# Optimization experiments

Hardware: AMD Instinct MI355X
Metric: run time of the kernel (lower is better)

Reference implementation:

```python
import jax, jax.numpy as jnp
import numpy as np
from functools import partial

D_MODEL = 1024
D_STATE = 16
D_CONV = 4
EXPAND = 2
DIM = EXPAND * D_MODEL  # 2048


def setup_inputs() -> dict:
    key = jax.random.key(0)
    ks = jax.random.split(key, 10)
    s = lambda fan_in: 1.0 / np.sqrt(fan_in)
    inp = {
        "x": jax.random.normal(ks[0], (8, 2048, D_MODEL), dtype=jnp.float32),
        "W_in": jax.random.normal(ks[1], (DIM, D_MODEL), dtype=jnp.float32) * s(D_MODEL),
        "b_in": jnp.zeros((DIM,), dtype=jnp.float32),
        "conv_w": jax.random.normal(ks[2], (DIM, 1, D_CONV), dtype=jnp.float32) * s(D_CONV),
        "conv_b": jnp.zeros((DIM,), dtype=jnp.float32),
        "W_x": jax.random.normal(ks[3], (3 * D_STATE, DIM), dtype=jnp.float32) * s(DIM),
        "W_dt": jax.random.normal(ks[4], (DIM, D_STATE), dtype=jnp.float32) * s(D_STATE),
        "b_dt": jnp.zeros((DIM,), dtype=jnp.float32),
        "W_out": jax.random.normal(ks[5], (D_MODEL, DIM), dtype=jnp.float32) * s(DIM),
        "b_out": jnp.zeros((D_MODEL,), dtype=jnp.float32),
    }
    return inp


def _selective_scan(xc, delta, A, Bm, Cm):
    # xc, delta: (B, L, DIM); Bm, Cm: (B, L, N); A: (N,)
    Bsz = xc.shape[0]
    h0 = jnp.zeros((Bsz, DIM, D_STATE), dtype=xc.dtype)

    def step(h, inputs):
        xc_t, d_t, b_t, c_t = inputs  # (B,DIM),(B,DIM),(B,N),(B,N)
        h = h * jnp.exp(d_t[:, :, None] * A) + xc_t[:, :, None] * b_t[:, None, :]
        y_t = jnp.einsum("bdn,bn->bd", h, c_t)
        return h, y_t

    tm = lambda a: jnp.swapaxes(a, 0, 1)  # time-major
    _, ys = jax.lax.scan(step, h0, (tm(xc), tm(delta), tm(Bm), tm(Cm)))
    return jnp.swapaxes(ys, 0, 1)  # (B, L, DIM)


def reference(x, W_in, b_in, conv_w, conv_b, W_x, W_dt, b_dt, W_out, b_out):
    A = -jnp.exp(jnp.linspace(0.0, -5.0, D_STATE).astype(x.dtype))  # (N,)
    xp = x @ W_in.T + b_in  # (B, L, DIM)
    # depthwise conv1d, padding=D_CONV-1 on BOTH sides (as torch Conv1d) -> length L+D_CONV-1
    xc = jax.lax.conv_general_dilated(
        jnp.swapaxes(xp, 1, 2), conv_w,
        window_strides=(1,), padding=[(D_CONV - 1, D_CONV - 1)],
        feature_group_count=DIM,
        dimension_numbers=("NCH", "OIH", "NCH"),
    ) + conv_b[None, :, None]
    xc = jnp.swapaxes(xc, 1, 2)  # (B, Lc, DIM)
    x_dbl = xc @ W_x.T  # (B, Lc, 3N)
    d_raw, Bm, Cm = jnp.split(x_dbl, [D_STATE, 2 * D_STATE], axis=-1)
    delta = jax.nn.softplus(d_raw @ W_dt.T + b_dt)  # (B, Lc, DIM)
    y = _selective_scan(xc, delta, A, Bm, Cm)  # (B, Lc, DIM)
    return y @ W_out.T + b_out  # (B, Lc, D_MODEL)
```

## Files before the change

kernel.cpp:

```cpp
#include <hip/hip_runtime.h>
#include <cstdint>
#include <cstddef>

#define B8 8
#define LSEQ 2048
#define LC 2051
#define DMODEL 1024
#define DIM 2048
#define LPAD 2054
#define M2 16408
#define M2P 16512
#define CS 32
#define NCH 65

typedef __attribute__((ext_vector_type(8))) short short8;
typedef __attribute__((ext_vector_type(4))) float floatx4;
typedef __attribute__((ext_vector_type(2))) float float2v;

__device__ __constant__ float AeT[16] = {
  -1.0f,          -0.71653131f, -0.51341712f, -0.36787944f,
  -0.26359714f,   -0.18887560f, -0.13533528f, -0.09697208f,
  -0.06948345f,   -0.04978707f, -0.03567399f, -0.02556154f,
  -0.01831564f,   -0.01312373f, -0.00940356f, -0.00673795f};

#define LOG2E 1.44269504088896f

__device__ __forceinline__ float bf2f(unsigned short h) {
  union { unsigned int u; float f; } v; v.u = ((unsigned int)h) << 16; return v.f;
}
__device__ __forceinline__ unsigned short f2bf(float f) {
  union { float f; unsigned int u; } v; v.f = f;
  unsigned int r = (v.u + 0x7FFFu + ((v.u >> 16) & 1u)) >> 16;
  return (unsigned short)r;
}

__device__ __forceinline__ float2v pk_mul_vv(float2v a, float2v b) {
  float2v d; asm("v_pk_mul_f32 %0, %1, %2" : "=v"(d) : "v"(a), "v"(b)); return d;
}
__device__ __forceinline__ float2v pk_mul_sv(float2v bs, float2v a) {
  float2v d; asm("v_pk_mul_f32 %0, %1, %2" : "=v"(d) : "s"(bs), "v"(a)); return d;
}
__device__ __forceinline__ float2v pk_fma_vvv(float2v a, float2v b, float2v c) {
  float2v d; asm("v_pk_fma_f32 %0, %1, %2, %3" : "=v"(d) : "v"(a), "v"(b), "v"(c)); return d;
}
__device__ __forceinline__ float2v pk_fma_vsv(float2v a, float2v bs, float2v c) {
  float2v d; asm("v_pk_fma_f32 %0, %1, %2, %3" : "=v"(d) : "v"(a), "s"(bs), "v"(c)); return d;
}
__device__ __forceinline__ float2v pk_add_vv(float2v a, float2v b) {
  float2v d; asm("v_pk_add_f32 %0, %1, %2" : "=v"(d) : "v"(a), "v"(b)); return d;
}
__device__ __forceinline__ float exp2_raw(float x) {
  float d; asm("v_exp_f32 %0, %1" : "=v"(d) : "v"(x)); return d;
}

__global__ __launch_bounds__(256) void cvt_f32_bf16(const float* __restrict__ in,
                                                    unsigned short* __restrict__ out,
                                                    int n8) {
  int i = blockIdx.x * 256 + threadIdx.x;
  if (i >= n8) return;
  const float4* p = (const float4*)in + (size_t)i * 2;
  float4 a = p[0], b = p[1];
  uint4 o;
  o.x = (unsigned)f2bf(a.x) | ((unsigned)f2bf(a.y) << 16);
  o.y = (unsigned)f2bf(a.z) | ((unsigned)f2bf(a.w) << 16);
  o.z = (unsigned)f2bf(b.x) | ((unsigned)f2bf(b.y) << 16);
  o.w = (unsigned)f2bf(b.z) | ((unsigned)f2bf(b.w) << 16);
  *((uint4*)out + i) = o;
}

__global__ __launch_bounds__(256) void zero_pads(unsigned short* __restrict__ xp) {
  int i = blockIdx.x * 256 + threadIdx.x;
  int b = i / 1536;
  int r6 = (i % 1536) / 256;
  int dd = (i % 256) * 8;
  int row = (r6 < 3) ? r6 : (2048 + r6);
  uint4 z = make_uint4(0, 0, 0, 0);
  *(uint4*)(xp + ((size_t)b * LPAD + row) * DIM + dd) = z;
}

__global__ __launch_bounds__(256) void conv_kernel(const unsigned short* __restrict__ xp,
                                                   const float* __restrict__ conv_w,
                                                   const float* __restrict__ conv_b,
                                                   unsigned short* __restrict__ xc) {
  const int tc = blockIdx.x, b = blockIdx.y;
  const int d0 = threadIdx.x * 8;
  const unsigned short* base = xp + ((size_t)b * LPAD + tc) * DIM + d0;

  float4 cw[8];
#pragma unroll
  for (int j = 0; j < 8; ++j) cw[j] = *(const float4*)(conv_w + (size_t)(d0 + j) * 4);

  float acc[8];
  const float4* cb4 = (const float4*)(conv_b + d0);
  float4 cb0 = cb4[0], cb1 = cb4[1];
  acc[0] = cb0.x; acc[1] = cb0.y; acc[2] = cb0.z; acc[3] = cb0.w;
  acc[4] = cb1.x; acc[5] = cb1.y; acc[6] = cb1.z; acc[7] = cb1.w;

#pragma unroll
  for (int k = 0; k < 4; ++k) {
    uint4 v = *(const uint4*)(base + (size_t)k * DIM);
    unsigned short e[8];
    e[0] = v.x & 0xffff; e[1] = v.x >> 16; e[2] = v.y & 0xffff; e[3] = v.y >> 16;
    e[4] = v.z & 0xffff; e[5] = v.z >> 16; e[6] = v.w & 0xffff; e[7] = v.w >> 16;
#pragma unroll
    for (int j = 0; j < 8; ++j)
      acc[j] = fmaf(bf2f(e[j]), ((const float*)&cw[j])[k], acc[j]);
  }
  uint4 o;
  o.x = (unsigned)f2bf(acc[0]) | ((unsigned)f2bf(acc[1]) << 16);
  o.y = (unsigned)f2bf(acc[2]) | ((unsigned)f2bf(acc[3]) << 16);
  o.z = (unsigned)f2bf(acc[4]) | ((unsigned)f2bf(acc[5]) << 16);
  o.w = (unsigned)f2bf(acc[6]) | ((unsigned)f2bf(acc[7]) << 16);
  *(uint4*)(xc + ((size_t)b * LC + tc) * DIM + d0) = o;
}

#define GAS(p) ((const __attribute__((address_space(1))) void*)(p))
#define LAS(p) ((__attribute__((address_space(3))) void*)(p))

template <int MODE, int NBM, int NBN, int LX>
__global__ __launch_bounds__(256) void gemm_bt(const unsigned short* __restrict__ A,
                                               const unsigned short* __restrict__ Bw,
                                               const float* __restrict__ bias,
                                               void* __restrict__ Cout, int K) {
  const int gid = blockIdx.x;
  const int xcd = gid & 7;
  const int j = gid >> 3;
  const int bm = xcd * LX + (j % LX);
  const int bn = j / LX;
  if (bm >= NBM) return;

  __shared__ __align__(16) unsigned short As[128 * 64];
  __shared__ __align__(16) unsigned short Bs[128 * 64];
  const int tid = threadIdx.x;
  const int lane = tid & 63, wave = tid >> 6;
  const int wr = wave >> 1, wc = wave & 1;

  floatx4 acc[4][4];
#pragma unroll
  for (int i = 0; i < 4; ++i)
#pragma unroll
    for (int j2 = 0; j2 < 4; ++j2) acc[i][j2] = (floatx4){0.f, 0.f, 0.f, 0.f};

  const int srow = tid >> 3;
  const int scol = ((tid & 7) ^ ((tid >> 3) & 7)) * 8;
  const unsigned short* Ab[4];
  const unsigned short* Bb[4];
#pragma unroll
  for (int L = 0; L < 4; ++L) {
    Ab[L] = A  + (size_t)(bm * 128 + L * 32 + srow) * K + scol;
    Bb[L] = Bw + (size_t)(bn * 128 + L * 32 + srow) * K + scol;
  }

  const int fr = lane & 15;
  const int hi = lane >> 4;
  const int fx = fr & 7;

  for (int k0 = 0; k0 < K; k0 += 64) {
    __syncthreads();
#pragma unroll
    for (int L = 0; L < 4; ++L) {
      __builtin_amdgcn_global_load_lds(GAS(Ab[L] + k0), LAS(As + L * 2048 + tid * 8), 16, 0, 0);
      __builtin_amdgcn_global_load_lds(GAS(Bb[L] + k0), LAS(Bs + L * 2048 + tid * 8), 16, 0, 0);
    }
    __syncthreads();

#pragma unroll
    for (int kk = 0; kk < 2; ++kk) {
      const int pb = ((kk * 4 + hi) ^ fx) * 8;
      short8 af[4], bf[4];
#pragma unroll
      for (int mt = 0; mt < 4; ++mt) af[mt] = *(const short8*)&As[(wr * 64 + mt * 16 + fr) * 64 + pb];
#pragma unroll
      for (int nt = 0; nt < 4; ++nt) bf[nt] = *(const short8*)&Bs[(wc * 64 + nt * 16 + fr) * 64 + pb];
#pragma unroll
      for (int mt = 0; mt < 4; ++mt)
#pragma unroll
        for (int nt = 0; nt < 4; ++nt)
          acc[mt][nt] = __builtin_amdgcn_mfma_f32_16x16x32_bf16(af[mt], bf[nt], acc[mt][nt], 0, 0, 0);
    }
  }

  const int er = (lane >> 4) * 4, ec = lane & 15;
#pragma unroll
  for (int mt = 0; mt < 4; ++mt) {
#pragma unroll
    for (int nt = 0; nt < 4; ++nt) {
#pragma unroll
      for (int i = 0; i < 4; ++i) {
        int r = bm * 128 + wr * 64 + mt * 16 + er + i;
        int c = bn * 128 + wc * 64 + nt * 16 + ec;
        float v = acc[mt][nt][i];
        if constexpr (MODE == 0) {
          int bb = r >> 11, t = r & 2047;
          ((unsigned short*)Cout)[((size_t)bb * LPAD + 3 + t) * DIM + c] = f2bf(v + bias[c]);
        } else if constexpr (MODE == 1) {
          if (r < M2 && c < 48) ((float*)Cout)[(size_t)r * 48 + c] = v;
        } else {
          if (r < M2) ((float*)Cout)[(size_t)r * DMODEL + c] = v + bias[c];
        }
      }
    }
  }
}

__global__ __launch_bounds__(256) void delta_kernel(const float* __restrict__ xdbl,
                                                    const float* __restrict__ W_dt,
                                                    const float* __restrict__ b_dt,
                                                    unsigned short* __restrict__ delta) {
  const int d = blockIdx.y * 256 + threadIdx.x;
  const int r0 = blockIdx.x * 8;
  float wv[16];
  const float4* wp = (const float4*)(W_dt + (size_t)d * 16);
#pragma unroll
  for (int q = 0; q < 4; ++q) {
    float4 t = wp[q];
    wv[q * 4 + 0] = t.x; wv[q * 4 + 1] = t.y; wv[q * 4 + 2] = t.z; wv[q * 4 + 3] = t.w;
  }
  const float bd = b_dt[d];
#pragma unroll
  for (int j = 0; j < 8; ++j) {
    const float* dr = xdbl + (size_t)(r0 + j) * 48;
    float z0 = bd, z1 = 0.f, z2 = 0.f, z3 = 0.f;
#pragma unroll
    for (int n = 0; n < 16; n += 4) {
      z0 = fmaf(dr[n + 0], wv[n + 0], z0);
      z1 = fmaf(dr[n + 1], wv[n + 1], z1);
      z2 = fmaf(dr[n + 2], wv[n + 2], z2);
      z3 = fmaf(dr[n + 3], wv[n + 3], z3);
    }
    float z = (z0 + z1) + (z2 + z3);
    float dl = (z > 20.f) ? z : __logf(1.f + __expf(z));
    delta[(size_t)(r0 + j) * DIM + d] = f2bf(dl);
  }
}

__global__ __launch_bounds__(256) void scan_pass1(const unsigned short* __restrict__ xc,
                                                  const unsigned short* __restrict__ dl,
                                                  const float* __restrict__ xd,
                                                  unsigned short* __restrict__ sdbuf,
                                                  unsigned short* __restrict__ qbuf) {
  const int wid = __builtin_amdgcn_readfirstlane((int)(threadIdx.x >> 6));
  const int lane = threadIdx.x & 63;
  const int W = blockIdx.x * 4 + wid;
  const int dg = W & 31;
  const int rest = W >> 5;
  const int c = rest % NCH;
  const int b = rest / NCH;
  const int d = dg * 64 + lane;
  const int t0 = c * CS;
  const int nst = (t0 + CS <= LC) ? CS : (LC - t0);

  float2v A2L[8];
#pragma unroll
  for (int i = 0; i < 8; ++i)
    A2L[i] = (float2v){AeT[2 * i] * LOG2E, AeT[2 * i + 1] * LOG2E};

  float2v h2[8];
#pragma unroll
  for (int i = 0; i < 8; ++i) h2[i] = (float2v){0.f, 0.f};
  float sumd = 0.f;

  const size_t row0 = (size_t)b * LC + t0;
  const float* xdb = xd + row0 * 48 + 16;
  const unsigned short* xcp = xc + row0 * DIM + d;
  const unsigned short* dp  = dl + row0 * DIM + d;

  float2v BA[8], BB[8];
#pragma unroll
  for (int j = 0; j < 8; ++j) BA[j] = *(const float2v*)(xdb + 2 * j);
  float d0v = bf2f(dp[0]), x0v = bf2f(xcp[0]);

  auto step = [&](const float2v (&Bv)[8], float dlt, float xcv) {
    sumd += dlt;
    float2v dlt2 = (float2v){dlt, dlt};
    float2v xcv2 = (float2v){xcv, xcv};
#pragma unroll
    for (int i = 0; i < 8; ++i) {
      float2v arg = pk_mul_vv(dlt2, A2L[i]);
      float e0 = exp2_raw(arg.x), e1 = exp2_raw(arg.y);
      float2v e2 = (float2v){e0, e1};
      h2[i] = pk_fma_vvv(h2[i], e2, pk_mul_sv(Bv[i], xcv2));
    }
  };

  for (int s = 0; s < nst; s += 2) {
    int s1 = (s + 1 < nst) ? s + 1 : s;
#pragma unroll
    for (int j = 0; j < 8; ++j) BB[j] = *(const float2v*)(xdb + (size_t)s1 * 48 + 2 * j);
    float d1v = bf2f(dp[(size_t)s1 * DIM]);
    float x1v = bf2f(xcp[(size_t)s1 * DIM]);
    step(BA, d0v, x0v);
    if (s + 1 >= nst) break;
    int s2 = (s + 2 < nst) ? s + 2 : s + 1;
#pragma unroll
    for (int j = 0; j < 8; ++j) BA[j] = *(const float2v*)(xdb + (size_t)s2 * 48 + 2 * j);
    d0v = bf2f(dp[(size_t)s2 * DIM]);
    x0v = bf2f(xcp[(size_t)s2 * DIM]);
    step(BB, d1v, x1v);
  }

  sdbuf[((size_t)(b * NCH + c) << 11) + d] = f2bf(sumd);
  const size_t base = ((size_t)(b * NCH + c) * 16) * 2048 + d;
#pragma unroll
  for (int i = 0; i < 8; ++i) {
    qbuf[base + ((size_t)(2 * i) << 11)]     = f2bf(h2[i].x);
    qbuf[base + ((size_t)(2 * i + 1) << 11)] = f2bf(h2[i].y);
  }
}

__global__ __launch_bounds__(256) void scan_boundary(const unsigned short* __restrict__ sdbuf,
                                                     unsigned short* __restrict__ qbuf) {
  const int tid = threadIdx.x;
  const int n = tid >> 4;
  const int d = blockIdx.x * 16 + (tid & 15);
  const int b = blockIdx.y;
  const float aL = AeT[n] * LOG2E;
  float h = 0.f;
  for (int c = 0; c < NCH; ++c) {
    const size_t sbase = ((size_t)(b * NCH + c) << 11);
    const float sd = bf2f(sdbuf[sbase + d]);
    const size_t base = (sbase << 4) + ((size_t)n << 11) + d;
    const float qv = bf2f(qbuf[base]);
    const float Pv = exp2_raw(sd * aL);
    qbuf[base] = f2bf(h);
    h = fmaf(Pv, h, qv);
  }
}

__global__ __launch_bounds__(256) void scan_pass2(const unsigned short* __restrict__ xc,
                                                  const unsigned short* __restrict__ dl,
                                                  const float* __restrict__ xd,
                                                  const unsigned short* __restrict__ hinit,
                                                  unsigned short* __restrict__ y) {
  const int wid = __builtin_amdgcn_readfirstlane((int)(threadIdx.x >> 6));
  const int lane = threadIdx.x & 63;
  const int W = blockIdx.x * 4 + wid;
  const int dg = W & 31;
  const int rest = W >> 5;
  const int c = rest % NCH;
  const int b = rest / NCH;
  const int d = dg * 64 + lane;
  const int t0 = c * CS;
  const int nst = (t0 + CS <= LC) ? CS : (LC - t0);

  float2v A2L[8];
#pragma unroll
  for (int i = 0; i < 8; ++i)
    A2L[i] = (float2v){AeT[2 * i] * LOG2E, AeT[2 * i + 1] * LOG2E};

  const size_t base = ((size_t)(b * NCH + c) * 16) * 2048 + d;
  float2v h2[8];
#pragma unroll
  for (int i = 0; i < 8; ++i)
    h2[i] = (float2v){bf2f(hinit[base + ((size_t)(2 * i) << 11)]),
                      bf2f(hinit[base + ((size_t)(2 * i + 1) << 11)])};

  const size_t row0 = (size_t)b * LC + t0;
  const float* xdb = xd + row0 * 48 + 16;
  const unsigned short* xcp = xc + row0 * DIM + d;
  const unsigned short* dp  = dl + row0 * DIM + d;
  unsigned short* yp = y + row0 * DIM + d;

  float2v BA[8], CA[8], BB[8], CB[8];
#pragma unroll
  for (int j = 0; j < 8; ++j) {
    BA[j] = *(const float2v*)(xdb + 2 * j);
    CA[j] = *(const float2v*)(xdb + 16 + 2 * j);
  }
  float d0v = bf2f(dp[0]), x0v = bf2f(xcp[0]);

  auto step = [&](const float2v (&Bv)[8], const float2v (&Cv)[8], float dlt, float xcv, int s) {
    float2v dlt2 = (float2v){dlt, dlt};
    float2v xcv2 = (float2v){xcv, xcv};
    float2v y2[4];
#pragma unroll
    for (int i = 0; i < 4; ++i) y2[i] = (float2v){0.f, 0.f};
#pragma unroll
    for (int i = 0; i < 8; ++i) {
      float2v arg = pk_mul_vv(dlt2, A2L[i]);
      float e0 = exp2_raw(arg.x), e1 = exp2_raw(arg.y);
      float2v e2 = (float2v){e0, e1};
      h2[i] = pk_fma_vvv(h2[i], e2, pk_mul_sv(Bv[i], xcv2));
      y2[i & 3] = pk_fma_vsv(h2[i], Cv[i], y2[i & 3]);
    }
    float2v s01 = pk_add_vv(y2[0], y2[1]);
    float2v s23 = pk_add_vv(y2[2], y2[3]);
    float2v st = pk_add_vv(s01, s23);
    yp[(size_t)s * DIM] = f2bf(st.x + st.y);
  };

  for (int s = 0; s < nst; s += 2) {
    int s1 = (s + 1 < nst) ? s + 1 : s;
#pragma unroll
    for (int j = 0; j < 8; ++j) {
      BB[j] = *(const float2v*)(xdb + (size_t)s1 * 48 + 2 * j);
      CB[j] = *(const float2v*)(xdb + (size_t)s1 * 48 + 16 + 2 * j);
    }
    float d1v = bf2f(dp[(size_t)s1 * DIM]);
    float x1v = bf2f(xcp[(size_t)s1 * DIM]);
    step(BA, CA, d0v, x0v, s);
    if (s + 1 >= nst) break;
    int s2 = (s + 2 < nst) ? s + 2 : s + 1;
#pragma unroll
    for (int j = 0; j < 8; ++j) {
      BA[j] = *(const float2v*)(xdb + (size_t)s2 * 48 + 2 * j);
      CA[j] = *(const float2v*)(xdb + (size_t)s2 * 48 + 16 + 2 * j);
    }
    d0v = bf2f(dp[(size_t)s2 * DIM]);
    x0v = bf2f(xcp[(size_t)s2 * DIM]);
    step(BB, CB, d1v, x1v, s + 1);
  }
}

extern "C" void kernel_launch(void* const* d_in, const int* in_sizes, int n_in,
                              void* d_out, int out_size, void* d_ws, size_t ws_size,
                              hipStream_t stream) {
  const float* x      = (const float*)d_in[0];
  const float* W_in   = (const float*)d_in[1];
  const float* b_in   = (const float*)d_in[2];
  const float* conv_w = (const float*)d_in[3];
  const float* conv_b = (const float*)d_in[4];
  const float* W_x    = (const float*)d_in[5];
  const float* W_dt   = (const float*)d_in[6];
  const float* b_dt   = (const float*)d_in[7];
  const float* W_out  = (const float*)d_in[8];
  const float* b_out  = (const float*)d_in[9];

  char* w = (char*)d_ws;
  unsigned short* xp    = (unsigned short*)w;
  unsigned short* delta = (unsigned short*)w;
  unsigned short* ybuf  = (unsigned short*)w;
  size_t off = (size_t)M2P * DIM * 2;
  unsigned short* xcb  = (unsigned short*)(w + off); off += (size_t)M2P * DIM * 2;
  size_t xA_off = off;
  unsigned short* xA   = (unsigned short*)(w + off); off += (size_t)16384 * 1024 * 2;
  unsigned short* wInB = (unsigned short*)(w + off); off += (size_t)2048 * 1024 * 2;
  unsigned short* wOutB= (unsigned short*)(w + off); off += (size_t)1024 * 2048 * 2;
  unsigned short* wXB  = (unsigned short*)(w + off); off += (size_t)128 * 2048 * 2;
  float* xdbl          = (float*)(w + off);          off += (size_t)M2 * 48 * 4;
  unsigned short* sdbuf = (unsigned short*)(w + xA_off);
  unsigned short* qbuf  = (unsigned short*)(w + xA_off + (size_t)B8 * NCH * 2048 * 2);
  (void)ws_size; (void)in_sizes; (void)n_in; (void)out_size;

  cvt_f32_bf16<<<8192, 256, 0, stream>>>(x, xA, 2097152);
  cvt_f32_bf16<<<1024, 256, 0, stream>>>(W_in, wInB, 262144);
  cvt_f32_bf16<<<1024, 256, 0, stream>>>(W_out, wOutB, 262144);
  cvt_f32_bf16<<<48,   256, 0, stream>>>(W_x, wXB, 12288);
  zero_pads<<<48, 256, 0, stream>>>(xp);

  gemm_bt<0, 128, 16, 16><<<2048, 256, 0, stream>>>(xA, wInB, b_in, xp, 1024);
  conv_kernel<<<dim3(LC, B8), 256, 0, stream>>>(xp, conv_w, conv_b, xcb);
  gemm_bt<1, 129, 1, 17><<<136, 256, 0, stream>>>(xcb, wXB, nullptr, xdbl, 2048);
  delta_kernel<<<dim3(2051, 8), 256, 0, stream>>>(xdbl, W_dt, b_dt, delta);

  scan_pass1<<<4160, 256, 0, stream>>>(xcb, delta, xdbl, sdbuf, qbuf);
  scan_boundary<<<dim3(128, B8), 256, 0, stream>>>(sdbuf, qbuf);
  scan_pass2<<<4160, 256, 0, stream>>>(xcb, delta, xdbl, qbuf, ybuf);

  gemm_bt<2, 129, 8, 17><<<1088, 256, 0, stream>>>(ybuf, wOutB, b_out, (float*)d_out, 2048);
}
```

Before: 579.6 us.

## Slide conv window over 16 rows, fully unroll scan chunks, add GEMM tail mapping

The depthwise conv kernel now has each block process 16 consecutive time rows, reusing the loaded rows in a sliding register window. This cuts redundant loads to one per output row instead of four and reduces block count. Both scan passes drop manual double-buffered prefetch in favour of a fully unrolled 32-step loop for full chunks, leaving load scheduling to the compiler. The GEMM gets a TAIL mode that maps the leftover M-block row onto a compact tail of the grid, removing idle blocks from the XCD-swizzled launch. The unroll may raise register pressure in the scan kernels.

```diff
diff --git a/kernel.cpp b/kernel.cpp
--- a/kernel.cpp
+++ b/kernel.cpp
@@ -82,51 +82,81 @@
                                                    const float* __restrict__ conv_w,
                                                    const float* __restrict__ conv_b,
                                                    unsigned short* __restrict__ xc) {
-  const int tc = blockIdx.x, b = blockIdx.y;
+  const int tc0 = blockIdx.x * 16;
+  const int b = blockIdx.y;
   const int d0 = threadIdx.x * 8;
-  const unsigned short* base = xp + ((size_t)b * LPAD + tc) * DIM + d0;
 
   float4 cw[8];
 #pragma unroll
   for (int j = 0; j < 8; ++j) cw[j] = *(const float4*)(conv_w + (size_t)(d0 + j) * 4);
-
-  float acc[8];
-  const float4* cb4 = (const float4*)(conv_b + d0);
-  float4 cb0 = cb4[0], cb1 = cb4[1];
-  acc[0] = cb0.x; acc[1] = cb0.y; acc[2] = cb0.z; acc[3] = cb0.w;
-  acc[4] = cb1.x; acc[5] = cb1.y; acc[6] = cb1.z; acc[7] = cb1.w;
-
-#pragma unroll
-  for (int k = 0; k < 4; ++k) {
-    uint4 v = *(const uint4*)(base + (size_t)k * DIM);
-    unsigned short e[8];
-    e[0] = v.x & 0xffff; e[1] = v.x >> 16; e[2] = v.y & 0xffff; e[3] = v.y >> 16;
-    e[4] = v.z & 0xffff; e[5] = v.z >> 16; e[6] = v.w & 0xffff; e[7] = v.w >> 16;
-#pragma unroll
-    for (int j = 0; j < 8; ++j)
-      acc[j] = fmaf(bf2f(e[j]), ((const float*)&cw[j])[k], acc[j]);
-  }
-  uint4 o;
-  o.x = (unsigned)f2bf(acc[0]) | ((unsigned)f2bf(acc[1]) << 16);
-  o.y = (unsigned)f2bf(acc[2]) | ((unsigned)f2bf(acc[3]) << 16);
-  o.z = (unsigned)f2bf(acc[4]) | ((unsigned)f2bf(acc[5]) << 16);
-  o.w = (unsigned)f2bf(acc[6]) | ((unsigned)f2bf(acc[7]) << 16);
-  *(uint4*)(xc + ((size_t)b * LC + tc) * DIM + d0) = o;
+  float cb[8];
+  {
+    const float4* cb4 = (const float4*)(conv_b + d0);
+    float4 c0 = cb4[0], c1 = cb4[1];
+    cb[0] = c0.x; cb[1] = c0.y; cb[2] = c0.z; cb[3] = c0.w;
+    cb[4] = c1.x; cb[5] = c1.y; cb[6] = c1.z; cb[7] = c1.w;
+  }
+
+  const unsigned short* base = xp + ((size_t)b * LPAD + tc0) * DIM + d0;
+  unsigned short* outp = xc + ((size_t)b * LC + tc0) * DIM + d0;
+
+  auto loadrow = [&](float (&w)[8], int r) {
+    uint4 v = *(const uint4*)(base + (size_t)r * DIM);
+    w[0] = bf2f(v.x & 0xffff); w[1] = bf2f(v.x >> 16);
+    w[2] = bf2f(v.y & 0xffff); w[3] = bf2f(v.y >> 16);
+    w[4] = bf2f(v.z & 0xffff); w[5] = bf2f(v.z >> 16);
+    w[6] = bf2f(v.w & 0xffff); w[7] = bf2f(v.w >> 16);
+  };
+
+  float wa[8], wb[8], wc[8];
+  loadrow(wa, 0); loadrow(wb, 1); loadrow(wc, 2);
+#pragma unroll
+  for (int i = 0; i < 16; ++i) {
+    float wd[8];
+    loadrow(wd, i + 3);
+    if (tc0 + i < LC) {
+      float acc[8];
+#pragma unroll
+      for (int j = 0; j < 8; ++j) {
+        acc[j] = cb[j];
+        acc[j] = fmaf(wa[j], cw[j].x, acc[j]);
+        acc[j] = fmaf(wb[j], cw[j].y, acc[j]);
+        acc[j] = fmaf(wc[j], cw[j].z, acc[j]);
+        acc[j] = fmaf(wd[j], cw[j].w, acc[j]);
+      }
+      uint4 o;
+      o.x = (unsigned)f2bf(acc[0]) | ((unsigned)f2bf(acc[1]) << 16);
+      o.y = (unsigned)f2bf(acc[2]) | ((unsigned)f2bf(acc[3]) << 16);
+      o.z = (unsigned)f2bf(acc[4]) | ((unsigned)f2bf(acc[5]) << 16);
+      o.w = (unsigned)f2bf(acc[6]) | ((unsigned)f2bf(acc[7]) << 16);
+      *(uint4*)(outp + (size_t)i * DIM) = o;
+    }
+#pragma unroll
+    for (int j = 0; j < 8; ++j) { wa[j] = wb[j]; wb[j] = wc[j]; wc[j] = wd[j]; }
+  }
 }
 
 #define GAS(p) ((const __attribute__((address_space(1))) void*)(p))
 #define LAS(p) ((__attribute__((address_space(3))) void*)(p))
 
-template <int MODE, int NBM, int NBN, int LX>
+template <int MODE, int NBM, int NBN, int LX, int TAIL>
 __global__ __launch_bounds__(256) void gemm_bt(const unsigned short* __restrict__ A,
                                                const unsigned short* __restrict__ Bw,
                                                const float* __restrict__ bias,
                                                void* __restrict__ Cout, int K) {
   const int gid = blockIdx.x;
-  const int xcd = gid & 7;
-  const int j = gid >> 3;
-  const int bm = xcd * LX + (j % LX);
-  const int bn = j / LX;
+  const int mainBlocks = 8 * LX * NBN;
+  int bm, bn;
+  if (TAIL && gid >= mainBlocks) {
+    const int e = gid - mainBlocks;
+    bm = 8 * LX + e / NBN;
+    bn = e % NBN;
+  } else {
+    const int xcd = gid & 7;
+    const int j = gid >> 3;
+    bm = xcd * LX + (j % LX);
+    bn = j / LX;
+  }
   if (bm >= NBM) return;
 
   __shared__ __align__(16) unsigned short As[128 * 64];
@@ -265,12 +295,12 @@
   const unsigned short* xcp = xc + row0 * DIM + d;
   const unsigned short* dp  = dl + row0 * DIM + d;
 
-  float2v BA[8], BB[8];
-#pragma unroll
-  for (int j = 0; j < 8; ++j) BA[j] = *(const float2v*)(xdb + 2 * j);
-  float d0v = bf2f(dp[0]), x0v = bf2f(xcp[0]);
-
-  auto step = [&](const float2v (&Bv)[8], float dlt, float xcv) {
+  auto body = [&](int s) {
+    float2v Bv[8];
+#pragma unroll
+    for (int j = 0; j < 8; ++j) Bv[j] = *(const float2v*)(xdb + (size_t)s * 48 + 2 * j);
+    float dlt = bf2f(dp[(size_t)s * DIM]);
+    float xcv = bf2f(xcp[(size_t)s * DIM]);
     sumd += dlt;
     float2v dlt2 = (float2v){dlt, dlt};
     float2v xcv2 = (float2v){xcv, xcv};
@@ -283,20 +313,11 @@
     }
   };
 
-  for (int s = 0; s < nst; s += 2) {
-    int s1 = (s + 1 < nst) ? s + 1 : s;
-#pragma unroll
-    for (int j = 0; j < 8; ++j) BB[j] = *(const float2v*)(xdb + (size_t)s1 * 48 + 2 * j);
-    float d1v = bf2f(dp[(size_t)s1 * DIM]);
-    float x1v = bf2f(xcp[(size_t)s1 * DIM]);
-    step(BA, d0v, x0v);
-    if (s + 1 >= nst) break;
-    int s2 = (s + 2 < nst) ? s + 2 : s + 1;
-#pragma unroll
-    for (int j = 0; j < 8; ++j) BA[j] = *(const float2v*)(xdb + (size_t)s2 * 48 + 2 * j);
-    d0v = bf2f(dp[(size_t)s2 * DIM]);
-    x0v = bf2f(xcp[(size_t)s2 * DIM]);
-    step(BB, d1v, x1v);
+  if (nst == CS) {
+#pragma unroll
+    for (int s = 0; s < CS; ++s) body(s);
+  } else {
+    for (int s = 0; s < nst; ++s) body(s);
   }
 
   sdbuf[((size_t)(b * NCH + c) << 11) + d] = f2bf(sumd);
@@ -361,15 +382,15 @@
   const unsigned short* dp  = dl + row0 * DIM + d;
   unsigned short* yp = y + row0 * DIM + d;
 
-  float2v BA[8], CA[8], BB[8], CB[8];
-#pragma unroll
-  for (int j = 0; j < 8; ++j) {
-    BA[j] = *(const float2v*)(xdb + 2 * j);
-    CA[j] = *(const float2v*)(xdb + 16 + 2 * j);
-  }
-  float d0v = bf2f(dp[0]), x0v = bf2f(xcp[0]);
-
-  auto step = [&](const float2v (&Bv)[8], const float2v (&Cv)[8], float dlt, float xcv, int s) {
+  auto body = [&](int s) {
+    float2v Bv[8], Cv[8];
+#pragma unroll
+    for (int j = 0; j < 8; ++j) {
+      Bv[j] = *(const float2v*)(xdb + (size_t)s * 48 + 2 * j);
+      Cv[j] = *(const float2v*)(xdb + (size_t)s * 48 + 16 + 2 * j);
+    }
+    float dlt = bf2f(dp[(size_t)s * DIM]);
+    float xcv = bf2f(xcp[(size_t)s * DIM]);
     float2v dlt2 = (float2v){dlt, dlt};
     float2v xcv2 = (float2v){xcv, xcv};
     float2v y2[4];
@@ -389,26 +410,11 @@
     yp[(size_t)s * DIM] = f2bf(st.x + st.y);
   };
 
-  for (int s = 0; s < nst; s += 2) {
-    int s1 = (s + 1 < nst) ? s + 1 : s;
-#pragma unroll
-    for (int j = 0; j < 8; ++j) {
-      BB[j] = *(const float2v*)(xdb + (size_t)s1 * 48 + 2 * j);
-      CB[j] = *(const float2v*)(xdb + (size_t)s1 * 48 + 16 + 2 * j);
-    }
-    float d1v = bf2f(dp[(size_t)s1 * DIM]);
-    float x1v = bf2f(xcp[(size_t)s1 * DIM]);
-    step(BA, CA, d0v, x0v, s);
-    if (s + 1 >= nst) break;
-    int s2 = (s + 2 < nst) ? s + 2 : s + 1;
-#pragma unroll
-    for (int j = 0; j < 8; ++j) {
-      BA[j] = *(const float2v*)(xdb + (size_t)s2 * 48 + 2 * j);
-      CA[j] = *(const float2v*)(xdb + (size_t)s2 * 48 + 16 + 2 * j);
-    }
-    d0v = bf2f(dp[(size_t)s2 * DIM]);
-    x0v = bf2f(xcp[(size_t)s2 * DIM]);
-    step(BB, CB, d1v, x1v, s + 1);
+  if (nst == CS) {
+#pragma unroll
+    for (int s = 0; s < CS; ++s) body(s);
+  } else {
+    for (int s = 0; s < nst; ++s) body(s);
   }
 }
 
@@ -448,14 +454,14 @@
   cvt_f32_bf16<<<48,   256, 0, stream>>>(W_x, wXB, 12288);
   zero_pads<<<48, 256, 0, stream>>>(xp);
 
-  gemm_bt<0, 128, 16, 16><<<2048, 256, 0, stream>>>(xA, wInB, b_in, xp, 1024);
-  conv_kernel<<<dim3(LC, B8), 256, 0, stream>>>(xp, conv_w, conv_b, xcb);
-  gemm_bt<1, 129, 1, 17><<<136, 256, 0, stream>>>(xcb, wXB, nullptr, xdbl, 2048);
+  gemm_bt<0, 128, 16, 16, 0><<<2048, 256, 0, stream>>>(xA, wInB, b_in, xp, 1024);
+  conv_kernel<<<dim3(129, B8), 256, 0, stream>>>(xp, conv_w, conv_b, xcb);
+  gemm_bt<1, 129, 1, 16, 1><<<129, 256, 0, stream>>>(xcb, wXB, nullptr, xdbl, 2048);
   delta_kernel<<<dim3(2051, 8), 256, 0, stream>>>(xdbl, W_dt, b_dt, delta);
 
   scan_pass1<<<4160, 256, 0, stream>>>(xcb, delta, xdbl, sdbuf, qbuf);
   scan_boundary<<<dim3(128, B8), 256, 0, stream>>>(sdbuf, qbuf);
   scan_pass2<<<4160, 256, 0, stream>>>(xcb, delta, xdbl, qbuf, ybuf);
 
-  gemm_bt<2, 129, 8, 17><<<1088, 256, 0, stream>>>(ybuf, wOutB, b_out, (float*)d_out, 2048);
-}
+  gemm_bt<2, 129, 8, 16, 1><<<1032, 256, 0, stream>>>(ybuf, wOutB, b_out, (float*)d_out, 2048);
+}
```

New measurement: 537.7 us. 7.2% less time.
